# Kernel optimization log

Measured on AMD Instinct MI355X. Metric: run time of the kernel, lower is better.

The kernel has to match this reference:

```python
import jax, jax.numpy as jnp
import numpy as np

N, F, H, ATTR = 128, 128, 8, 3
HU, HUE = [16, 8], [4, 2]


def setup_inputs() -> dict:
    key = jax.random.key(0)
    ks = iter(jax.random.split(key, 40))
    def g(shape):
        return jax.random.normal(next(ks), shape, dtype=jnp.float32) * 0.1
    M = N * N
    return dict(
        X=g((N, F)), A=g((ATTR, N, N)), E=g((ATTR, N, N)), e2n_adj=g((N, M)),
        Wn0=g((ATTR, H, F, HU[0])), bn0=jnp.zeros((ATTR, H, HU[0]), jnp.float32),
        an0_s=g((ATTR, H, HU[0])), an0_n=g((ATTR, H, HU[0])),
        Wn1=g((ATTR, H, H * HU[0], HU[1])), bn1=jnp.zeros((ATTR, H, HU[1]), jnp.float32),
        an1_s=g((ATTR, H, HU[1])), an1_n=g((ATTR, H, HU[1])),
        We0=g((H, ATTR, HUE[0])), be0=jnp.zeros((H, HUE[0]), jnp.float32),
        We1=g((H, H * HUE[0], HUE[1])), be1=jnp.zeros((H, HUE[1]), jnp.float32),
        Wct0=g((H, HU[0] + HUE[0], HU[0])), bct0=jnp.zeros((H, HU[0]), jnp.float32),
        Wct1=g((H, HU[1] + HUE[1], HU[1])), bct1=jnp.zeros((H, HU[1]), jnp.float32),
        ae0_s=g((H, HU[0])), ae0_n=g((H, HUE[0])),
        ae1_s=g((H, HU[1])), ae1_n=g((H, HUE[1])),
    )


def _leaky(x):
    return jnp.where(x >= 0, x, 0.2 * x)  # LeakyReLU(0.2)


def reference(X, A, E, e2n_adj,
              Wn0, bn0, an0_s, an0_n, Wn1, bn1, an1_s, an1_n,
              We0, be0, We1, be1, Wct0, bct0, Wct1, bct1,
              ae0_s, ae0_n, ae1_s, ae1_n):
    # Eval mode (dropout = identity). Heads are vectorized (leading h axis).
    nb_attr, n = E.shape[0], X.shape[0]
    E_e2n = E.reshape(nb_attr, -1).T  # [M, nb_attr], row-major flatten matches torch .view(-1,1)
    edge_layers = [(We0, be0, Wct0, bct0, ae0_s, ae0_n),
                   (We1, be1, Wct1, bct1, ae1_s, ae1_n)]
    attrs_out = []
    for attr in range(nb_attr):
        node_layers = [(Wn0[attr], bn0[attr], an0_s[attr], an0_n[attr]),
                       (Wn1[attr], bn1[attr], an1_s[attr], an1_n[attr])]
        X_head, X_edge, E_info = X, E_e2n, E[attr]
        h_list = [X]
        for (Wn, bn, an_s, an_n), (We, be, Wct, bct, ae_s, ae_n) in zip(node_layers, edge_layers):
            feat = jnp.einsum('nf,hfk->hnk', X_head, Wn)          # node features per head
            feat_e = jnp.einsum('mf,hfk->hmk', X_edge, We)        # edge features per head
            a_self = jnp.einsum('hnk,hk->hn', feat, ae_s)
            a_edge = jnp.einsum('hmk,hk->hm', feat_e, ae_n)
            # edge-to-node attention over all M = N*N edges
            alpha_e = jax.nn.softmax(_leaky(a_self[:, :, None] + a_edge[:, None, :]) + e2n_adj[None], axis=-1)
            nf_e = jnp.einsum('hnm,hmk->hnk', alpha_e, feat_e) + be[:, None, :]
            feat2 = jnp.einsum('hnc,hck->hnk', jnp.concatenate([feat, nf_e], axis=-1), Wct) + bct[:, None, :]
            s2 = jnp.einsum('hnk,hk->hn', feat2, an_s)
            n2 = jnp.einsum('hnk,hk->hn', feat2, an_n)
            dense = jnp.einsum('hij,jm->him', s2[:, :, None] + n2[:, None, :], E_info)  # [h,N,N]
            alpha = jax.nn.softmax(_leaky(dense) + A[attr][None], axis=-1)
            nf = jax.nn.elu(jnp.einsum('hnm,hmk->hnk', alpha, feat2) + bn[:, None, :])
            h1 = jnp.transpose(nf, (1, 0, 2)).reshape(n, -1)      # concat heads on feature axis
            h_list.append(h1)
            X_head = h1
            X_edge = jnp.transpose(feat_e, (1, 0, 2)).reshape(feat_e.shape[1], -1)
            E_info = alpha[-1]                                    # last head's attention matrix
        attrs_out.append(jnp.concatenate(h_list, axis=-1)[:, None, :])
    return jnp.concatenate(attrs_out, axis=1)                     # [N, nb_attr, F + 8*16 + 8*8]
```

## Files before the change

### kernel.cpp

```cpp
#include <hip/hip_runtime.h>

static constexpr int N = 128;
static constexpr int F = 128;
static constexpr int H = 8;
static constexpr int NATTR = 3;
static constexpr int M = N * N;
static constexpr int OUTW = 320;
static constexpr int MSL = 32;
static constexpr int CH = M / MSL;
static constexpr float LOG2E = 1.4426950408889634f;

__device__ __forceinline__ float leaky(float x) { return fmaxf(x, 0.2f * x); }

template <int KE, bool L1>
__global__ void __launch_bounds__(256)
k_ea(const float* __restrict__ E,
     const float* __restrict__ xsrc,
     int xStride,
     const float* __restrict__ Wn,
     const float* __restrict__ aes,
     const float* __restrict__ We0,
     const float* __restrict__ aen,
     const float* __restrict__ We1,
     const float* __restrict__ adj,
     float* __restrict__ part) {
    constexpr int KW = L1 ? 8 : 16;
    __shared__ __align__(16) float sFe[4 * CH * KE];
    __shared__ __align__(16) float sAe[4 * CH];
    __shared__ __align__(16) float sWv[12 * 128];
    __shared__ __align__(16) float sWc[48];

    int b = blockIdx.x;
    int ms = b & (MSL - 1);
    int nt = (b >> 5) & 7;
    int h0 = (b >> 8) * 4;
    int tid = threadIdx.x;
    int r = tid >> 4, l = tid & 15;
    int n = nt * 16 + r;
    int m0 = ms * CH;

    for (int idx = tid; idx < 12 * 128; idx += 256) {
        int c = idx >> 7, f = idx & 127;
        int a = c >> 2, h = h0 + (c & 3);
        const float* wp = Wn + ((size_t)(a * H + h) * F + f) * KW;
        const float* ap = aes + h * KW;
        float acc = 0.f;
#pragma unroll
        for (int k = 0; k < KW; ++k) acc += wp[k] * ap[k];
        sWv[idx] = acc * LOG2E;
    }
    if (L1) {
        if (tid < 24) {
            int hh = tid / 6, rem = tid % 6, at = rem >> 1, k2 = rem & 1;
            int h = h0 + hh;
            float acc = 0.f;
            for (int c = 0; c < 32; ++c)
                acc += We0[((c >> 2) * 3 + at) * 4 + (c & 3)] *
                       We1[(h * 32 + c) * 2 + k2];
            sWc[(hh * 3 + at) * 2 + k2] = acc;
        }
        __syncthreads();
    }
    for (int idx = tid; idx < 4 * CH; idx += 256) {
        int hh = idx >> 9, mm = idx & (CH - 1);
        int m = m0 + mm, h = h0 + hh;
        float e0 = E[m], e1 = E[M + m], e2 = E[2 * M + m];
        if (!L1) {
            float aa = 0.f;
#pragma unroll
            for (int k = 0; k < 4; ++k) {
                float f = e0 * We0[(h * 3 + 0) * 4 + k] +
                          e1 * We0[(h * 3 + 1) * 4 + k] +
                          e2 * We0[(h * 3 + 2) * 4 + k];
                sFe[(hh * CH + mm) * 4 + k] = f;
                aa += f * aen[h * 4 + k];
            }
            sAe[hh * CH + mm] = aa * LOG2E;
        } else {
            float f0 = e0 * sWc[(hh * 3 + 0) * 2 + 0] + e1 * sWc[(hh * 3 + 1) * 2 + 0] +
                       e2 * sWc[(hh * 3 + 2) * 2 + 0];
            float f1 = e0 * sWc[(hh * 3 + 0) * 2 + 1] + e1 * sWc[(hh * 3 + 1) * 2 + 1] +
                       e2 * sWc[(hh * 3 + 2) * 2 + 1];
            sFe[(hh * CH + mm) * 2 + 0] = f0;
            sFe[(hh * CH + mm) * 2 + 1] = f1;
            sAe[hh * CH + mm] = (f0 * aen[h * 2 + 0] + f1 * aen[h * 2 + 1]) * LOG2E;
        }
    }
    __syncthreads();

    float as[NATTR][4];
#pragma unroll
    for (int a = 0; a < NATTR; ++a) {
        const float* xr = xsrc + (size_t)a * xStride + (size_t)n * F;
        float xv[8];
#pragma unroll
        for (int j = 0; j < 8; ++j) xv[j] = xr[l + 16 * j];
#pragma unroll
        for (int hh = 0; hh < 4; ++hh) {
            const float* wr = sWv + (a * 4 + hh) * 128;
            float d = 0.f;
#pragma unroll
            for (int j = 0; j < 8; ++j) d += xv[j] * wr[l + 16 * j];
#pragma unroll
            for (int off = 1; off < 16; off <<= 1) d += __shfl_xor(d, off);
            as[a][hh] = d;
        }
    }

    float sum[4][NATTR];
    float acc[4][NATTR][KE];
#pragma unroll
    for (int hh = 0; hh < 4; ++hh)
#pragma unroll
        for (int a = 0; a < NATTR; ++a) {
            sum[hh][a] = 0.f;
#pragma unroll
            for (int k = 0; k < KE; ++k) acc[hh][a][k] = 0.f;
        }

    const float* adjp = adj + (size_t)n * M + m0;
    for (int i = l * 4; i < CH; i += 64) {
        const float4 av = *(const float4*)(adjp + i);
        float4 ev[4];
#pragma unroll
        for (int hh = 0; hh < 4; ++hh)
            ev[hh] = *(const float4*)&sAe[hh * CH + i];
#pragma unroll
        for (int j = 0; j < 4; ++j) {
            float adjv = (&av.x)[j] * LOG2E;
#pragma unroll
            for (int hh = 0; hh < 4; ++hh) {
                float aev = (&ev[hh].x)[j];
                float fv[KE];
                if (KE == 4) {
                    const float4 fq = *(const float4*)&sFe[(hh * CH + i + j) * 4];
                    fv[0] = fq.x; fv[1] = fq.y; fv[2] = fq.z; fv[3] = fq.w;
                } else {
                    const float2 fq = *(const float2*)&sFe[(hh * CH + i + j) * 2];
                    fv[0] = fq.x; fv[1] = fq.y;
                }
#pragma unroll
                for (int a = 0; a < NATTR; ++a) {
                    float t = as[a][hh] + aev;
                    float p = __builtin_amdgcn_exp2f(fmaxf(t, 0.2f * t) + adjv);
                    sum[hh][a] += p;
#pragma unroll
                    for (int k = 0; k < KE; ++k) acc[hh][a][k] += p * fv[k];
                }
            }
        }
    }

#pragma unroll
    for (int off = 1; off < 16; off <<= 1) {
#pragma unroll
        for (int hh = 0; hh < 4; ++hh)
#pragma unroll
            for (int a = 0; a < NATTR; ++a) {
                sum[hh][a] += __shfl_xor(sum[hh][a], off);
#pragma unroll
                for (int k = 0; k < KE; ++k) acc[hh][a][k] += __shfl_xor(acc[hh][a][k], off);
            }
    }
    if (l == 0) {
#pragma unroll
        for (int hh = 0; hh < 4; ++hh)
#pragma unroll
            for (int a = 0; a < NATTR; ++a) {
                float* pp = part + (((size_t)(a * H + h0 + hh) * N + n) * MSL + ms) * 8;
#pragma unroll
                for (int k = 0; k < KE; ++k) pp[k] = acc[hh][a][k];
                pp[7] = sum[hh][a];
            }
    }
}

template <int K, int KE, bool FIRST>
__global__ void __launch_bounds__(256)
k_mid(const float* __restrict__ xsrc,
      int xStride,
      const float* __restrict__ Wn,
      const float* __restrict__ part,
      const float* __restrict__ be,
      const float* __restrict__ Wct,
      const float* __restrict__ bct,
      const float* __restrict__ ans,
      const float* __restrict__ ann,
      const float* __restrict__ X,
      float* __restrict__ out,
      float* __restrict__ feat2,
      float* __restrict__ s2,
      float* __restrict__ n2) {
    constexpr int CIN = K + KE;
    __shared__ __align__(16) float sWn[F * K];
    __shared__ __align__(16) float sW[CIN * K];
    __shared__ __align__(16) float sIn[32 * CIN];
    __shared__ __align__(16) float sF2[32 * K];

    int b = blockIdx.x;
    int nt = b & 3, h = (b >> 2) & 7, a = b >> 5;
    int n0 = nt * 32;
    int tid = threadIdx.x;

    for (int i = tid; i < F * K; i += 256)
        sWn[i] = Wn[(size_t)(a * H + h) * F * K + i];
    for (int i = tid; i < CIN * K; i += 256) sW[i] = Wct[h * CIN * K + i];

    {
        int r = tid >> 3, g = tid & 7;
        int n = n0 + r;
        const float* pp = part + ((size_t)(a * H + h) * N + n) * MSL * 8;
        float av[4] = {0.f, 0.f, 0.f, 0.f};
        float sv = 0.f;
        for (int ms = g; ms < MSL; ms += 8) {
            const float4 x = *(const float4*)(pp + ms * 8);
            const float4 y = *(const float4*)(pp + ms * 8 + 4);
            av[0] += x.x; av[1] += x.y;
            if (KE == 4) { av[2] += x.z; av[3] += x.w; }
            sv += y.w;
        }
#pragma unroll
        for (int off = 1; off < 8; off <<= 1) {
#pragma unroll
            for (int k = 0; k < KE; ++k) av[k] += __shfl_xor(av[k], off);
            sv += __shfl_xor(sv, off);
        }
        if (g == 0) {
            float inv = 1.f / sv;
#pragma unroll
            for (int k = 0; k < KE; ++k)
                sIn[r * CIN + K + k] = av[k] * inv + be[h * KE + k];
        }
    }
    if (FIRST && h == 0) {
        for (int i = tid; i < 32 * F; i += 256) {
            int n = n0 + (i >> 7);
            int f = i & (F - 1);
            out[(n * NATTR + a) * OUTW + f] = X[n * F + f];
        }
    }
    __syncthreads();

    for (int o = tid; o < 32 * K; o += 256) {
        int r = o / K, k = o % K;
        const float* xr = xsrc + (size_t)a * xStride + (size_t)(n0 + r) * F;
        float acc = 0.f;
        for (int f = 0; f < F; ++f) acc += xr[f] * sWn[f * K + k];
        sIn[r * CIN + k] = acc;
    }
    __syncthreads();

    for (int o = tid; o < 32 * K; o += 256) {
        int r = o / K, k = o % K;
        float acc = bct[h * K + k];
        for (int c = 0; c < CIN; ++c) acc += sIn[r * CIN + c] * sW[c * K + k];
        sF2[o] = acc;
        feat2[((size_t)(a * H + h) * N + n0 + r) * 16 + k] = acc;
    }
    __syncthreads();
    if (tid < 32) {
        int r = tid;
        float ss = 0.f, nn = 0.f;
        for (int k = 0; k < K; ++k) {
            ss += sF2[r * K + k] * ans[(a * H + h) * K + k];
            nn += sF2[r * K + k] * ann[(a * H + h) * K + k];
        }
        s2[(a * H + h) * N + n0 + r] = ss;
        n2[(a * H + h) * N + n0 + r] = nn;
    }
}

template <int K, bool FIRST>
__global__ void __launch_bounds__(256)
k_node(const float* __restrict__ feat2,
       const float* __restrict__ s2,
       const float* __restrict__ n2,
       const float* __restrict__ Einfo,
       const float* __restrict__ Amat,
       const float* __restrict__ bn,
       float* __restrict__ out, int outOff,
       float* __restrict__ xh_out,
       float* __restrict__ einfo_out) {
    __shared__ __align__(16) float sF2[N * K];
    __shared__ __align__(16) float sS2[N];
    __shared__ __align__(16) float sn2[N];
    __shared__ __align__(16) float sdE[N];
    __shared__ __align__(16) float scE[N];
    __shared__ __align__(16) float sAlpha[4 * N];
    __shared__ __align__(16) float sRed[256];

    int b = blockIdx.x;
    int itile = b & 7, h = (b >> 3) & 7, a = b >> 6;
    int tid = threadIdx.x;

    for (int i = tid; i < N * K; i += 256)
        sF2[i] = feat2[((size_t)(a * H + h) * N + i / K) * 16 + i % K];
    if (tid < N) {
        sS2[tid] = s2[(a * H + h) * N + tid];
        sn2[tid] = n2[(a * H + h) * N + tid];
    }
    __syncthreads();

    {
        int m = tid & 127, w = tid >> 7;
        const float* Ep = Einfo + (size_t)a * M;
        float dacc = 0.f, cacc = 0.f;
        for (int j = w * 64; j < w * 64 + 64; ++j) {
            float v = Ep[j * N + m];
            dacc += sn2[j] * v;
            cacc += v;
        }
        sRed[tid] = dacc;
        sAlpha[w * N + m] = cacc;
        __syncthreads();
        if (tid < N) {
            sdE[tid] = sRed[tid] + sRed[128 + tid];
            scE[tid] = sAlpha[tid] + sAlpha[N + tid];
        }
    }
    __syncthreads();

    for (int pass = 0; pass < 4; ++pass) {
        int r = tid >> 6;
        int lane = tid & 63;
        int i = itile * 16 + pass * 4 + r;
        float s = sS2[i];
        const float* Ap = Amat + ((size_t)a * N + i) * N;
        float v0 = leaky(s * scE[lane] + sdE[lane]) + Ap[lane];
        float v1 = leaky(s * scE[lane + 64] + sdE[lane + 64]) + Ap[lane + 64];
        float p0 = __expf(v0), p1 = __expf(v1);
        float ssum = p0 + p1;
#pragma unroll
        for (int off = 1; off < 64; off <<= 1) ssum += __shfl_xor(ssum, off);
        float inv = 1.f / ssum;
        float a0 = p0 * inv, a1 = p1 * inv;
        sAlpha[r * N + lane] = a0;
        sAlpha[r * N + lane + 64] = a1;
        if (FIRST && h == H - 1) {
            einfo_out[((size_t)a * N + i) * N + lane] = a0;
            einfo_out[((size_t)a * N + i) * N + lane + 64] = a1;
        }
        __syncthreads();
        {
            int rr = tid >> 6, g = (tid >> 4) & 3, k = tid & 15;
            float acc = 0.f;
            if (k < K) {
                for (int it = 0; it < 32; ++it) {
                    int mm = g + 4 * it;
                    acc += sAlpha[rr * N + mm] * sF2[mm * K + k];
                }
            }
            sRed[tid] = acc;
        }
        __syncthreads();
        {
            int rr = tid >> 6, k = tid & 63;
            if (k < K) {
                float tot = bn[(a * H + h) * K + k];
#pragma unroll
                for (int g = 0; g < 4; ++g) tot += sRed[rr * 64 + g * 16 + k];
                float e = tot > 0.f ? tot : __expf(tot) - 1.f;
                int i2 = itile * 16 + pass * 4 + rr;
                out[(i2 * NATTR + a) * OUTW + outOff + h * K + k] = e;
                if (FIRST)
                    xh_out[((size_t)a * N + i2) * F + h * K + k] = e;
            }
        }
        __syncthreads();
    }
}

extern "C" void kernel_launch(void* const* d_in, const int* in_sizes, int n_in,
                              void* d_out, int out_size, void* d_ws, size_t ws_size,
                              hipStream_t stream) {
    const float* X    = (const float*)d_in[0];
    const float* A    = (const float*)d_in[1];
    const float* E    = (const float*)d_in[2];
    const float* adj  = (const float*)d_in[3];
    const float* Wn0  = (const float*)d_in[4];
    const float* bn0  = (const float*)d_in[5];
    const float* an0s = (const float*)d_in[6];
    const float* an0n = (const float*)d_in[7];
    const float* Wn1  = (const float*)d_in[8];
    const float* bn1  = (const float*)d_in[9];
    const float* an1s = (const float*)d_in[10];
    const float* an1n = (const float*)d_in[11];
    const float* We0  = (const float*)d_in[12];
    const float* be0  = (const float*)d_in[13];
    const float* We1  = (const float*)d_in[14];
    const float* be1  = (const float*)d_in[15];
    const float* Wct0 = (const float*)d_in[16];
    const float* bct0 = (const float*)d_in[17];
    const float* Wct1 = (const float*)d_in[18];
    const float* bct1 = (const float*)d_in[19];
    const float* ae0s = (const float*)d_in[20];
    const float* ae0n = (const float*)d_in[21];
    const float* ae1s = (const float*)d_in[22];
    const float* ae1n = (const float*)d_in[23];
    float* out = (float*)d_out;

    float* p = (float*)d_ws;
    float* part  = p; p += (size_t)NATTR * H * N * MSL * 8;
    float* feat2 = p; p += NATTR * H * N * 16;
    float* s2b   = p; p += NATTR * H * N;
    float* n2b   = p; p += NATTR * H * N;
    float* einfo = p; p += NATTR * N * N;
    float* xh    = p; p += NATTR * N * F;

    k_ea<4, false><<<dim3(512), dim3(256), 0, stream>>>(
        E, X, 0, Wn0, ae0s, We0, ae0n, nullptr, adj, part);
    k_mid<16, 4, true><<<dim3(96), dim3(256), 0, stream>>>(
        X, 0, Wn0, part, be0, Wct0, bct0, an0s, an0n, X, out,
        feat2, s2b, n2b);
    k_node<16, true><<<dim3(192), dim3(256), 0, stream>>>(
        feat2, s2b, n2b, E, A, bn0, out, F, xh, einfo);

    k_ea<2, true><<<dim3(512), dim3(256), 0, stream>>>(
        E, xh, N * F, Wn1, ae1s, We0, ae1n, We1, adj, part);
    k_mid<8, 2, false><<<dim3(96), dim3(256), 0, stream>>>(
        xh, N * F, Wn1, part, be1, Wct1, bct1, an1s, an1n, nullptr, nullptr,
        feat2, s2b, n2b);
    k_node<8, false><<<dim3(192), dim3(256), 0, stream>>>(
        feat2, s2b, n2b, einfo, A, bn1, out, F + 128, nullptr, nullptr);
}
```

Baseline: 86.29 us.

## Split edge-attention over more m-slices and fewer heads per block, swizzle LDS

After: 89.89 us. 4.2% more time.

```diff
diff --git a/kernel.cpp b/kernel.cpp
--- a/kernel.cpp
+++ b/kernel.cpp
@@ -6,11 +6,14 @@
 static constexpr int NATTR = 3;
 static constexpr int M = N * N;
 static constexpr int OUTW = 320;
-static constexpr int MSL = 32;
+static constexpr int MSL = 64;
 static constexpr int CH = M / MSL;
+static constexpr int HG = 2;
 static constexpr float LOG2E = 1.4426950408889634f;
 
 __device__ __forceinline__ float leaky(float x) { return fmaxf(x, 0.2f * x); }
+__device__ __forceinline__ int swz4(int s) { return s ^ ((s >> 3) & 7); }
+__device__ __forceinline__ int swz2(int s) { return s ^ ((s >> 4) & 3); }
 
 template <int KE, bool L1>
 __global__ void __launch_bounds__(256)
@@ -25,23 +28,23 @@
      const float* __restrict__ adj,
      float* __restrict__ part) {
     constexpr int KW = L1 ? 8 : 16;
-    __shared__ __align__(16) float sFe[4 * CH * KE];
-    __shared__ __align__(16) float sAe[4 * CH];
-    __shared__ __align__(16) float sWv[12 * 128];
-    __shared__ __align__(16) float sWc[48];
+    __shared__ __align__(16) float sFe[HG * CH * KE];
+    __shared__ __align__(16) float sAe[HG * CH];
+    __shared__ __align__(16) float sWv[NATTR * HG * 128];
+    __shared__ __align__(16) float sWc[HG * 3 * 2];
 
     int b = blockIdx.x;
     int ms = b & (MSL - 1);
-    int nt = (b >> 5) & 7;
-    int h0 = (b >> 8) * 4;
+    int nt = (b >> 6) & 7;
+    int h0 = (b >> 9) * HG;
     int tid = threadIdx.x;
     int r = tid >> 4, l = tid & 15;
     int n = nt * 16 + r;
     int m0 = ms * CH;
 
-    for (int idx = tid; idx < 12 * 128; idx += 256) {
+    for (int idx = tid; idx < NATTR * HG * 128; idx += 256) {
         int c = idx >> 7, f = idx & 127;
-        int a = c >> 2, h = h0 + (c & 3);
+        int a = c / HG, h = h0 + (c % HG);
         const float* wp = Wn + ((size_t)(a * H + h) * F + f) * KW;
         const float* ap = aes + h * KW;
         float acc = 0.f;
@@ -50,7 +53,7 @@
         sWv[idx] = acc * LOG2E;
     }
     if (L1) {
-        if (tid < 24) {
+        if (tid < HG * 6) {
             int hh = tid / 6, rem = tid % 6, at = rem >> 1, k2 = rem & 1;
             int h = h0 + hh;
             float acc = 0.f;
@@ -61,34 +64,38 @@
         }
         __syncthreads();
     }
-    for (int idx = tid; idx < 4 * CH; idx += 256) {
-        int hh = idx >> 9, mm = idx & (CH - 1);
-        int m = m0 + mm, h = h0 + hh;
+    for (int mm = tid; mm < CH; mm += 256) {
+        int m = m0 + mm;
         float e0 = E[m], e1 = E[M + m], e2 = E[2 * M + m];
-        if (!L1) {
-            float aa = 0.f;
-#pragma unroll
-            for (int k = 0; k < 4; ++k) {
-                float f = e0 * We0[(h * 3 + 0) * 4 + k] +
-                          e1 * We0[(h * 3 + 1) * 4 + k] +
-                          e2 * We0[(h * 3 + 2) * 4 + k];
-                sFe[(hh * CH + mm) * 4 + k] = f;
-                aa += f * aen[h * 4 + k];
-            }
-            sAe[hh * CH + mm] = aa * LOG2E;
-        } else {
-            float f0 = e0 * sWc[(hh * 3 + 0) * 2 + 0] + e1 * sWc[(hh * 3 + 1) * 2 + 0] +
-                       e2 * sWc[(hh * 3 + 2) * 2 + 0];
-            float f1 = e0 * sWc[(hh * 3 + 0) * 2 + 1] + e1 * sWc[(hh * 3 + 1) * 2 + 1] +
-                       e2 * sWc[(hh * 3 + 2) * 2 + 1];
-            sFe[(hh * CH + mm) * 2 + 0] = f0;
-            sFe[(hh * CH + mm) * 2 + 1] = f1;
-            sAe[hh * CH + mm] = (f0 * aen[h * 2 + 0] + f1 * aen[h * 2 + 1]) * LOG2E;
-        }
-    }
-    __syncthreads();
-
-    float as[NATTR][4];
+#pragma unroll
+        for (int hh = 0; hh < HG; ++hh) {
+            int h = h0 + hh;
+            if (!L1) {
+                float4 v;
+                float aa = 0.f;
+#pragma unroll
+                for (int k = 0; k < 4; ++k) {
+                    float f = e0 * We0[(h * 3 + 0) * 4 + k] +
+                              e1 * We0[(h * 3 + 1) * 4 + k] +
+                              e2 * We0[(h * 3 + 2) * 4 + k];
+                    (&v.x)[k] = f;
+                    aa += f * aen[h * 4 + k];
+                }
+                *(float4*)&sFe[(hh * CH + swz4(mm)) * 4] = v;
+                sAe[hh * CH + mm] = aa * LOG2E;
+            } else {
+                float f0 = e0 * sWc[(hh * 3 + 0) * 2 + 0] + e1 * sWc[(hh * 3 + 1) * 2 + 0] +
+                           e2 * sWc[(hh * 3 + 2) * 2 + 0];
+                float f1 = e0 * sWc[(hh * 3 + 0) * 2 + 1] + e1 * sWc[(hh * 3 + 1) * 2 + 1] +
+                           e2 * sWc[(hh * 3 + 2) * 2 + 1];
+                *(float2*)&sFe[(hh * CH + swz2(mm)) * 2] = make_float2(f0, f1);
+                sAe[hh * CH + mm] = (f0 * aen[h * 2 + 0] + f1 * aen[h * 2 + 1]) * LOG2E;
+            }
+        }
+    }
+    __syncthreads();
+
+    float as[NATTR][HG];
 #pragma unroll
     for (int a = 0; a < NATTR; ++a) {
         const float* xr = xsrc + (size_t)a * xStride + (size_t)n * F;
@@ -96,8 +103,8 @@
 #pragma unroll
         for (int j = 0; j < 8; ++j) xv[j] = xr[l + 16 * j];
 #pragma unroll
-        for (int hh = 0; hh < 4; ++hh) {
-            const float* wr = sWv + (a * 4 + hh) * 128;
+        for (int hh = 0; hh < HG; ++hh) {
+            const float* wr = sWv + (a * HG + hh) * 128;
             float d = 0.f;
 #pragma unroll
             for (int j = 0; j < 8; ++j) d += xv[j] * wr[l + 16 * j];
@@ -107,10 +114,10 @@
         }
     }
 
-    float sum[4][NATTR];
-    float acc[4][NATTR][KE];
-#pragma unroll
-    for (int hh = 0; hh < 4; ++hh)
+    float sum[HG][NATTR];
+    float acc[HG][NATTR][KE];
+#pragma unroll
+    for (int hh = 0; hh < HG; ++hh)
 #pragma unroll
         for (int a = 0; a < NATTR; ++a) {
             sum[hh][a] = 0.f;
@@ -121,22 +128,22 @@
     const float* adjp = adj + (size_t)n * M + m0;
     for (int i = l * 4; i < CH; i += 64) {
         const float4 av = *(const float4*)(adjp + i);
-        float4 ev[4];
-#pragma unroll
-        for (int hh = 0; hh < 4; ++hh)
+        float4 ev[HG];
+#pragma unroll
+        for (int hh = 0; hh < HG; ++hh)
             ev[hh] = *(const float4*)&sAe[hh * CH + i];
 #pragma unroll
         for (int j = 0; j < 4; ++j) {
             float adjv = (&av.x)[j] * LOG2E;
 #pragma unroll
-            for (int hh = 0; hh < 4; ++hh) {
+            for (int hh = 0; hh < HG; ++hh) {
                 float aev = (&ev[hh].x)[j];
                 float fv[KE];
                 if (KE == 4) {
-                    const float4 fq = *(const float4*)&sFe[(hh * CH + i + j) * 4];
+                    const float4 fq = *(const float4*)&sFe[(hh * CH + swz4(i + j)) * 4];
                     fv[0] = fq.x; fv[1] = fq.y; fv[2] = fq.z; fv[3] = fq.w;
                 } else {
-                    const float2 fq = *(const float2*)&sFe[(hh * CH + i + j) * 2];
+                    const float2 fq = *(const float2*)&sFe[(hh * CH + swz2(i + j)) * 2];
                     fv[0] = fq.x; fv[1] = fq.y;
                 }
 #pragma unroll
@@ -154,7 +161,7 @@
 #pragma unroll
     for (int off = 1; off < 16; off <<= 1) {
 #pragma unroll
-        for (int hh = 0; hh < 4; ++hh)
+        for (int hh = 0; hh < HG; ++hh)
 #pragma unroll
             for (int a = 0; a < NATTR; ++a) {
                 sum[hh][a] += __shfl_xor(sum[hh][a], off);
@@ -164,7 +171,7 @@
     }
     if (l == 0) {
 #pragma unroll
-        for (int hh = 0; hh < 4; ++hh)
+        for (int hh = 0; hh < HG; ++hh)
 #pragma unroll
             for (int a = 0; a < NATTR; ++a) {
                 float* pp = part + (((size_t)(a * H + h0 + hh) * N + n) * MSL + ms) * 8;
@@ -407,7 +414,7 @@
     float* einfo = p; p += NATTR * N * N;
     float* xh    = p; p += NATTR * N * F;
 
-    k_ea<4, false><<<dim3(512), dim3(256), 0, stream>>>(
+    k_ea<4, false><<<dim3((H / HG) * 8 * MSL), dim3(256), 0, stream>>>(
         E, X, 0, Wn0, ae0s, We0, ae0n, nullptr, adj, part);
     k_mid<16, 4, true><<<dim3(96), dim3(256), 0, stream>>>(
         X, 0, Wn0, part, be0, Wct0, bct0, an0s, an0n, X, out,
@@ -415,7 +422,7 @@
     k_node<16, true><<<dim3(192), dim3(256), 0, stream>>>(
         feat2, s2b, n2b, E, A, bn0, out, F, xh, einfo);
 
-    k_ea<2, true><<<dim3(512), dim3(256), 0, stream>>>(
+    k_ea<2, true><<<dim3((H / HG) * 8 * MSL), dim3(256), 0, stream>>>(
         E, xh, N * F, Wn1, ae1s, We0, ae1n, We1, adj, part);
     k_mid<8, 2, false><<<dim3(96), dim3(256), 0, stream>>>(
         xh, N * F, Wn1, part, be1, Wct1, bct1, an1s, an1n, nullptr, nullptr,
```

## Split self-attention precompute into prep kernel and remap edge-attention work per thread

Applied to the files above, without the earlier changes.

New measurement: 123.1 us. +42.7%, slower.

```diff
diff --git a/kernel.cpp b/kernel.cpp
--- a/kernel.cpp
+++ b/kernel.cpp
@@ -6,172 +6,132 @@
 static constexpr int NATTR = 3;
 static constexpr int M = N * N;
 static constexpr int OUTW = 320;
-static constexpr int MSL = 32;
+static constexpr int MSL = 256;
 static constexpr int CH = M / MSL;
 static constexpr float LOG2E = 1.4426950408889634f;
 
 __device__ __forceinline__ float leaky(float x) { return fmaxf(x, 0.2f * x); }
 
+template <int K>
+__global__ void __launch_bounds__(128)
+k_prep(const float* __restrict__ xsrc, int xStride,
+       const float* __restrict__ Wn,
+       const float* __restrict__ aes,
+       float* __restrict__ aself) {
+    int a = blockIdx.x / H, h = blockIdx.x % H;
+    __shared__ float wv[F];
+    int tid = threadIdx.x;
+    {
+        const float* wp = Wn + ((size_t)(a * H + h) * F + tid) * K;
+        const float* ap = aes + h * K;
+        float acc = 0.f;
+#pragma unroll
+        for (int k = 0; k < K; ++k) acc += wp[k] * ap[k];
+        wv[tid] = acc;
+    }
+    __syncthreads();
+    const float* xr = xsrc + (size_t)a * xStride + (size_t)tid * F;
+    float acc = 0.f;
+    for (int f = 0; f < F; ++f) acc += xr[f] * wv[f];
+    aself[(a * H + h) * N + tid] = acc * LOG2E;
+}
+
 template <int KE, bool L1>
-__global__ void __launch_bounds__(256)
+__global__ void __launch_bounds__(128)
 k_ea(const float* __restrict__ E,
-     const float* __restrict__ xsrc,
-     int xStride,
-     const float* __restrict__ Wn,
-     const float* __restrict__ aes,
+     const float* __restrict__ aself,
      const float* __restrict__ We0,
      const float* __restrict__ aen,
      const float* __restrict__ We1,
      const float* __restrict__ adj,
      float* __restrict__ part) {
-    constexpr int KW = L1 ? 8 : 16;
-    __shared__ __align__(16) float sFe[4 * CH * KE];
-    __shared__ __align__(16) float sAe[4 * CH];
-    __shared__ __align__(16) float sWv[12 * 128];
-    __shared__ __align__(16) float sWc[48];
-
     int b = blockIdx.x;
     int ms = b & (MSL - 1);
-    int nt = (b >> 5) & 7;
-    int h0 = (b >> 8) * 4;
+    int nt = b >> 8;
     int tid = threadIdx.x;
-    int r = tid >> 4, l = tid & 15;
+    int h = tid & 7, r = tid >> 3;
     int n = nt * 16 + r;
     int m0 = ms * CH;
 
-    for (int idx = tid; idx < 12 * 128; idx += 256) {
-        int c = idx >> 7, f = idx & 127;
-        int a = c >> 2, h = h0 + (c & 3);
-        const float* wp = Wn + ((size_t)(a * H + h) * F + f) * KW;
-        const float* ap = aes + h * KW;
-        float acc = 0.f;
-#pragma unroll
-        for (int k = 0; k < KW; ++k) acc += wp[k] * ap[k];
-        sWv[idx] = acc * LOG2E;
-    }
-    if (L1) {
-        if (tid < 24) {
-            int hh = tid / 6, rem = tid % 6, at = rem >> 1, k2 = rem & 1;
-            int h = h0 + hh;
-            float acc = 0.f;
-            for (int c = 0; c < 32; ++c)
-                acc += We0[((c >> 2) * 3 + at) * 4 + (c & 3)] *
-                       We1[(h * 32 + c) * 2 + k2];
-            sWc[(hh * 3 + at) * 2 + k2] = acc;
-        }
-        __syncthreads();
-    }
-    for (int idx = tid; idx < 4 * CH; idx += 256) {
-        int hh = idx >> 9, mm = idx & (CH - 1);
-        int m = m0 + mm, h = h0 + hh;
-        float e0 = E[m], e1 = E[M + m], e2 = E[2 * M + m];
-        if (!L1) {
-            float aa = 0.f;
-#pragma unroll
-            for (int k = 0; k < 4; ++k) {
-                float f = e0 * We0[(h * 3 + 0) * 4 + k] +
-                          e1 * We0[(h * 3 + 1) * 4 + k] +
-                          e2 * We0[(h * 3 + 2) * 4 + k];
-                sFe[(hh * CH + mm) * 4 + k] = f;
-                aa += f * aen[h * 4 + k];
-            }
-            sAe[hh * CH + mm] = aa * LOG2E;
-        } else {
-            float f0 = e0 * sWc[(hh * 3 + 0) * 2 + 0] + e1 * sWc[(hh * 3 + 1) * 2 + 0] +
-                       e2 * sWc[(hh * 3 + 2) * 2 + 0];
-            float f1 = e0 * sWc[(hh * 3 + 0) * 2 + 1] + e1 * sWc[(hh * 3 + 1) * 2 + 1] +
-                       e2 * sWc[(hh * 3 + 2) * 2 + 1];
-            sFe[(hh * CH + mm) * 2 + 0] = f0;
-            sFe[(hh * CH + mm) * 2 + 1] = f1;
-            sAe[hh * CH + mm] = (f0 * aen[h * 2 + 0] + f1 * aen[h * 2 + 1]) * LOG2E;
-        }
-    }
-    __syncthreads();
-
-    float as[NATTR][4];
+    float w[12];
+    float an[KE];
+    if (!L1) {
+#pragma unroll
+        for (int at = 0; at < 3; ++at)
+#pragma unroll
+            for (int k = 0; k < 4; ++k) w[at * 4 + k] = We0[(h * 3 + at) * 4 + k];
+#pragma unroll
+        for (int k = 0; k < 4; ++k) an[k] = aen[h * 4 + k] * LOG2E;
+    } else {
+#pragma unroll
+        for (int at = 0; at < 3; ++at)
+#pragma unroll
+            for (int k2 = 0; k2 < 2; ++k2) {
+                float acc = 0.f;
+                for (int c = 0; c < 32; ++c)
+                    acc += We0[((c >> 2) * 3 + at) * 4 + (c & 3)] *
+                           We1[(h * 32 + c) * 2 + k2];
+                w[at * 2 + k2] = acc;
+            }
+        an[0] = aen[h * 2 + 0] * LOG2E;
+        an[1] = aen[h * 2 + 1] * LOG2E;
+    }
+    float u[NATTR];
+#pragma unroll
+    for (int a = 0; a < NATTR; ++a) u[a] = aself[(a * H + h) * N + n];
+
+    float sum[NATTR];
+    float acc[NATTR][KE];
 #pragma unroll
     for (int a = 0; a < NATTR; ++a) {
-        const float* xr = xsrc + (size_t)a * xStride + (size_t)n * F;
-        float xv[8];
-#pragma unroll
-        for (int j = 0; j < 8; ++j) xv[j] = xr[l + 16 * j];
-#pragma unroll
-        for (int hh = 0; hh < 4; ++hh) {
-            const float* wr = sWv + (a * 4 + hh) * 128;
-            float d = 0.f;
-#pragma unroll
-            for (int j = 0; j < 8; ++j) d += xv[j] * wr[l + 16 * j];
-#pragma unroll
-            for (int off = 1; off < 16; off <<= 1) d += __shfl_xor(d, off);
-            as[a][hh] = d;
-        }
-    }
-
-    float sum[4][NATTR];
-    float acc[4][NATTR][KE];
-#pragma unroll
-    for (int hh = 0; hh < 4; ++hh)
-#pragma unroll
-        for (int a = 0; a < NATTR; ++a) {
-            sum[hh][a] = 0.f;
-#pragma unroll
-            for (int k = 0; k < KE; ++k) acc[hh][a][k] = 0.f;
-        }
+        sum[a] = 0.f;
+#pragma unroll
+        for (int k = 0; k < KE; ++k) acc[a][k] = 0.f;
+    }
 
     const float* adjp = adj + (size_t)n * M + m0;
-    for (int i = l * 4; i < CH; i += 64) {
-        const float4 av = *(const float4*)(adjp + i);
-        float4 ev[4];
-#pragma unroll
-        for (int hh = 0; hh < 4; ++hh)
-            ev[hh] = *(const float4*)&sAe[hh * CH + i];
+    for (int i = 0; i < CH; i += 4) {
+        const float4 aq = *(const float4*)(adjp + i);
+        const float4 e0 = *(const float4*)(E + m0 + i);
+        const float4 e1 = *(const float4*)(E + M + m0 + i);
+        const float4 e2 = *(const float4*)(E + 2 * M + m0 + i);
 #pragma unroll
         for (int j = 0; j < 4; ++j) {
-            float adjv = (&av.x)[j] * LOG2E;
-#pragma unroll
-            for (int hh = 0; hh < 4; ++hh) {
-                float aev = (&ev[hh].x)[j];
-                float fv[KE];
-                if (KE == 4) {
-                    const float4 fq = *(const float4*)&sFe[(hh * CH + i + j) * 4];
-                    fv[0] = fq.x; fv[1] = fq.y; fv[2] = fq.z; fv[3] = fq.w;
-                } else {
-                    const float2 fq = *(const float2*)&sFe[(hh * CH + i + j) * 2];
-                    fv[0] = fq.x; fv[1] = fq.y;
+            float x0 = (&e0.x)[j], x1 = (&e1.x)[j], x2 = (&e2.x)[j];
+            float fe[KE];
+            float v = 0.f;
+            if (KE == 4) {
+#pragma unroll
+                for (int k = 0; k < 4; ++k) {
+                    fe[k] = x0 * w[k] + x1 * w[4 + k] + x2 * w[8 + k];
+                    v += fe[k] * an[k];
                 }
-#pragma unroll
-                for (int a = 0; a < NATTR; ++a) {
-                    float t = as[a][hh] + aev;
-                    float p = __builtin_amdgcn_exp2f(fmaxf(t, 0.2f * t) + adjv);
-                    sum[hh][a] += p;
-#pragma unroll
-                    for (int k = 0; k < KE; ++k) acc[hh][a][k] += p * fv[k];
-                }
-            }
-        }
-    }
-
-#pragma unroll
-    for (int off = 1; off < 16; off <<= 1) {
-#pragma unroll
-        for (int hh = 0; hh < 4; ++hh)
+            } else {
+                fe[0] = x0 * w[0] + x1 * w[2] + x2 * w[4];
+                fe[1] = x0 * w[1] + x1 * w[3] + x2 * w[5];
+                v = fe[0] * an[0] + fe[1] * an[1];
+            }
+            float adjv = (&aq.x)[j] * LOG2E;
 #pragma unroll
             for (int a = 0; a < NATTR; ++a) {
-                sum[hh][a] += __shfl_xor(sum[hh][a], off);
-#pragma unroll
-                for (int k = 0; k < KE; ++k) acc[hh][a][k] += __shfl_xor(acc[hh][a][k], off);
-            }
-    }
-    if (l == 0) {
-#pragma unroll
-        for (int hh = 0; hh < 4; ++hh)
-#pragma unroll
-            for (int a = 0; a < NATTR; ++a) {
-                float* pp = part + (((size_t)(a * H + h0 + hh) * N + n) * MSL + ms) * 8;
-#pragma unroll
-                for (int k = 0; k < KE; ++k) pp[k] = acc[hh][a][k];
-                pp[7] = sum[hh][a];
-            }
+                float t = u[a] + v;
+                float p = __builtin_amdgcn_exp2f(fmaxf(t, 0.2f * t) + adjv);
+                sum[a] += p;
+#pragma unroll
+                for (int k = 0; k < KE; ++k) acc[a][k] += p * fe[k];
+            }
+        }
+    }
+
+#pragma unroll
+    for (int a = 0; a < NATTR; ++a) {
+        float* pp = part + (((size_t)ms * NATTR + a) * N + n) * 64 + h * 8;
+        float4 x = make_float4(acc[a][0], acc[a][1],
+                               KE == 4 ? acc[a][2] : 0.f,
+                               KE == 4 ? acc[a][3] : 0.f);
+        float4 y = make_float4(0.f, 0.f, 0.f, sum[a]);
+        *(float4*)pp = x;
+        *(float4*)(pp + 4) = y;
     }
 }
 
@@ -209,12 +169,12 @@
     {
         int r = tid >> 3, g = tid & 7;
         int n = n0 + r;
-        const float* pp = part + ((size_t)(a * H + h) * N + n) * MSL * 8;
         float av[4] = {0.f, 0.f, 0.f, 0.f};
         float sv = 0.f;
         for (int ms = g; ms < MSL; ms += 8) {
-            const float4 x = *(const float4*)(pp + ms * 8);
-            const float4 y = *(const float4*)(pp + ms * 8 + 4);
+            const float* pp = part + (((size_t)ms * NATTR + a) * N + n) * 64 + h * 8;
+            const float4 x = *(const float4*)pp;
+            const float4 y = *(const float4*)(pp + 4);
             av[0] += x.x; av[1] += x.y;
             if (KE == 4) { av[2] += x.z; av[3] += x.w; }
             sv += y.w;
@@ -400,23 +360,26 @@
     float* out = (float*)d_out;
 
     float* p = (float*)d_ws;
-    float* part  = p; p += (size_t)NATTR * H * N * MSL * 8;
+    float* part  = p; p += (size_t)MSL * NATTR * N * 64;
+    float* aself = p; p += NATTR * H * N;
     float* feat2 = p; p += NATTR * H * N * 16;
     float* s2b   = p; p += NATTR * H * N;
     float* n2b   = p; p += NATTR * H * N;
     float* einfo = p; p += NATTR * N * N;
     float* xh    = p; p += NATTR * N * F;
 
-    k_ea<4, false><<<dim3(512), dim3(256), 0, stream>>>(
-        E, X, 0, Wn0, ae0s, We0, ae0n, nullptr, adj, part);
+    k_prep<16><<<dim3(24), dim3(128), 0, stream>>>(X, 0, Wn0, ae0s, aself);
+    k_ea<4, false><<<dim3(8 * MSL), dim3(128), 0, stream>>>(
+        E, aself, We0, ae0n, nullptr, adj, part);
     k_mid<16, 4, true><<<dim3(96), dim3(256), 0, stream>>>(
         X, 0, Wn0, part, be0, Wct0, bct0, an0s, an0n, X, out,
         feat2, s2b, n2b);
     k_node<16, true><<<dim3(192), dim3(256), 0, stream>>>(
         feat2, s2b, n2b, E, A, bn0, out, F, xh, einfo);
 
-    k_ea<2, true><<<dim3(512), dim3(256), 0, stream>>>(
-        E, xh, N * F, Wn1, ae1s, We0, ae1n, We1, adj, part);
+    k_prep<8><<<dim3(24), dim3(128), 0, stream>>>(xh, N * F, Wn1, ae1s, aself);
+    k_ea<2, true><<<dim3(8 * MSL), dim3(128), 0, stream>>>(
+        E, aself, We0, ae1n, We1, adj, part);
     k_mid<8, 2, false><<<dim3(96), dim3(256), 0, stream>>>(
         xh, N * F, Wn1, part, be1, Wct1, bct1, an1s, an1n, nullptr, nullptr,
         feat2, s2b, n2b);
```

## Factor edge softmax exponentials into precomputed exp terms to remove inner-loop exp

Applied to the files above, without the earlier changes.

Result: slower. 90.87 us (+5.3%).

```diff
diff --git a/kernel.cpp b/kernel.cpp
--- a/kernel.cpp
+++ b/kernel.cpp
@@ -11,6 +11,18 @@
 static constexpr float LOG2E = 1.4426950408889634f;
 
 __device__ __forceinline__ float leaky(float x) { return fmaxf(x, 0.2f * x); }
+
+__global__ void __launch_bounds__(256)
+k_expadj(const float* __restrict__ adj, float* __restrict__ expA) {
+    int i = (blockIdx.x * 256 + threadIdx.x) * 4;
+    float4 v = *(const float4*)(adj + i);
+    float4 r;
+    r.x = __builtin_amdgcn_exp2f(v.x * LOG2E);
+    r.y = __builtin_amdgcn_exp2f(v.y * LOG2E);
+    r.z = __builtin_amdgcn_exp2f(v.z * LOG2E);
+    r.w = __builtin_amdgcn_exp2f(v.w * LOG2E);
+    *(float4*)(expA + i) = r;
+}
 
 template <int KE, bool L1>
 __global__ void __launch_bounds__(256)
@@ -22,11 +34,12 @@
      const float* __restrict__ We0,
      const float* __restrict__ aen,
      const float* __restrict__ We1,
-     const float* __restrict__ adj,
+     const float* __restrict__ expA,
      float* __restrict__ part) {
     constexpr int KW = L1 ? 8 : 16;
     __shared__ __align__(16) float sFe[4 * CH * KE];
-    __shared__ __align__(16) float sAe[4 * CH];
+    __shared__ __align__(16) float sT1[4 * CH];
+    __shared__ __align__(16) float sT2[4 * CH];
     __shared__ __align__(16) float sWv[12 * 128];
     __shared__ __align__(16) float sWc[48];
 
@@ -65,8 +78,9 @@
         int hh = idx >> 9, mm = idx & (CH - 1);
         int m = m0 + mm, h = h0 + hh;
         float e0 = E[m], e1 = E[M + m], e2 = E[2 * M + m];
+        float aa;
         if (!L1) {
-            float aa = 0.f;
+            aa = 0.f;
 #pragma unroll
             for (int k = 0; k < 4; ++k) {
                 float f = e0 * We0[(h * 3 + 0) * 4 + k] +
@@ -75,7 +89,6 @@
                 sFe[(hh * CH + mm) * 4 + k] = f;
                 aa += f * aen[h * 4 + k];
             }
-            sAe[hh * CH + mm] = aa * LOG2E;
         } else {
             float f0 = e0 * sWc[(hh * 3 + 0) * 2 + 0] + e1 * sWc[(hh * 3 + 1) * 2 + 0] +
                        e2 * sWc[(hh * 3 + 2) * 2 + 0];
@@ -83,12 +96,15 @@
                        e2 * sWc[(hh * 3 + 2) * 2 + 1];
             sFe[(hh * CH + mm) * 2 + 0] = f0;
             sFe[(hh * CH + mm) * 2 + 1] = f1;
-            sAe[hh * CH + mm] = (f0 * aen[h * 2 + 0] + f1 * aen[h * 2 + 1]) * LOG2E;
-        }
-    }
-    __syncthreads();
-
-    float as[NATTR][4];
+            aa = f0 * aen[h * 2 + 0] + f1 * aen[h * 2 + 1];
+        }
+        float sv = aa * LOG2E;
+        sT1[hh * CH + mm] = __builtin_amdgcn_exp2f(sv);
+        sT2[hh * CH + mm] = __builtin_amdgcn_exp2f(0.2f * sv);
+    }
+    __syncthreads();
+
+    float EU1[NATTR][4], EU2[NATTR][4], RU1[NATTR][4];
 #pragma unroll
     for (int a = 0; a < NATTR; ++a) {
         const float* xr = xsrc + (size_t)a * xStride + (size_t)n * F;
@@ -103,7 +119,9 @@
             for (int j = 0; j < 8; ++j) d += xv[j] * wr[l + 16 * j];
 #pragma unroll
             for (int off = 1; off < 16; off <<= 1) d += __shfl_xor(d, off);
-            as[a][hh] = d;
+            EU1[a][hh] = __builtin_amdgcn_exp2f(d);
+            EU2[a][hh] = __builtin_amdgcn_exp2f(0.2f * d);
+            RU1[a][hh] = __builtin_amdgcn_exp2f(-d);
         }
     }
 
@@ -118,19 +136,22 @@
             for (int k = 0; k < KE; ++k) acc[hh][a][k] = 0.f;
         }
 
-    const float* adjp = adj + (size_t)n * M + m0;
+    const float* eAp = expA + (size_t)n * M + m0;
     for (int i = l * 4; i < CH; i += 64) {
-        const float4 av = *(const float4*)(adjp + i);
-        float4 ev[4];
-#pragma unroll
-        for (int hh = 0; hh < 4; ++hh)
-            ev[hh] = *(const float4*)&sAe[hh * CH + i];
+        const float4 eq = *(const float4*)(eAp + i);
+        float4 t1v[4], t2v[4];
+#pragma unroll
+        for (int hh = 0; hh < 4; ++hh) {
+            t1v[hh] = *(const float4*)&sT1[hh * CH + i];
+            t2v[hh] = *(const float4*)&sT2[hh * CH + i];
+        }
 #pragma unroll
         for (int j = 0; j < 4; ++j) {
-            float adjv = (&av.x)[j] * LOG2E;
+            float eAj = (&eq.x)[j];
 #pragma unroll
             for (int hh = 0; hh < 4; ++hh) {
-                float aev = (&ev[hh].x)[j];
+                float T1 = (&t1v[hh].x)[j];
+                float T2 = (&t2v[hh].x)[j];
                 float fv[KE];
                 if (KE == 4) {
                     const float4 fq = *(const float4*)&sFe[(hh * CH + i + j) * 4];
@@ -139,10 +160,13 @@
                     const float2 fq = *(const float2*)&sFe[(hh * CH + i + j) * 2];
                     fv[0] = fq.x; fv[1] = fq.y;
                 }
+                float tA1 = T1 * eAj;
+                float tA2 = T2 * eAj;
 #pragma unroll
                 for (int a = 0; a < NATTR; ++a) {
-                    float t = as[a][hh] + aev;
-                    float p = __builtin_amdgcn_exp2f(fmaxf(t, 0.2f * t) + adjv);
+                    float b1 = EU1[a][hh] * tA1;
+                    float b2 = EU2[a][hh] * tA2;
+                    float p = (T1 >= RU1[a][hh]) ? b1 : b2;
                     sum[hh][a] += p;
 #pragma unroll
                     for (int k = 0; k < KE; ++k) acc[hh][a][k] += p * fv[k];
@@ -400,6 +424,7 @@
     float* out = (float*)d_out;
 
     float* p = (float*)d_ws;
+    float* expA  = p; p += (size_t)N * M;
     float* part  = p; p += (size_t)NATTR * H * N * MSL * 8;
     float* feat2 = p; p += NATTR * H * N * 16;
     float* s2b   = p; p += NATTR * H * N;
@@ -407,8 +432,10 @@
     float* einfo = p; p += NATTR * N * N;
     float* xh    = p; p += NATTR * N * F;
 
+    k_expadj<<<dim3(N * M / 1024), dim3(256), 0, stream>>>(adj, expA);
+
     k_ea<4, false><<<dim3(512), dim3(256), 0, stream>>>(
-        E, X, 0, Wn0, ae0s, We0, ae0n, nullptr, adj, part);
+        E, X, 0, Wn0, ae0s, We0, ae0n, nullptr, expA, part);
     k_mid<16, 4, true><<<dim3(96), dim3(256), 0, stream>>>(
         X, 0, Wn0, part, be0, Wct0, bct0, an0s, an0n, X, out,
         feat2, s2b, n2b);
@@ -416,7 +443,7 @@
         feat2, s2b, n2b, E, A, bn0, out, F, xh, einfo);
 
     k_ea<2, true><<<dim3(512), dim3(256), 0, stream>>>(
-        E, xh, N * F, Wn1, ae1s, We0, ae1n, We1, adj, part);
+        E, xh, N * F, Wn1, ae1s, We0, ae1n, We1, expA, part);
     k_mid<8, 2, false><<<dim3(96), dim3(256), 0, stream>>>(
         xh, N * F, Wn1, part, be1, Wct1, bct1, an1s, an1n, nullptr, nullptr,
         feat2, s2b, n2b);
```
